# Performance work log

Hardware: AMD Instinct MI355X
Metric: run time of the kernel (lower is better)

The kernel has to match this reference:

```python
import jax, jax.numpy as jnp
import numpy as np

HEAD_SIZE = 64


def q_shift_multihead(x, ph, pw, head_dim=HEAD_SIZE, shift=1):
    # x: [B, T, C], T == ph*pw. Quarter-wise spatial shifts per head channel block.
    B, T, C = x.shape
    a = jnp.transpose(x, (0, 2, 1)).reshape(B, C // head_dim, head_dim, ph, pw)
    q = head_dim // 4
    out = jnp.zeros_like(a)
    out = out.at[:, :, 0:q, :, shift:].set(a[:, :, 0:q, :, :-shift])          # shift right in W
    out = out.at[:, :, q:2 * q, :, :-shift].set(a[:, :, q:2 * q, :, shift:])  # shift left in W
    out = out.at[:, :, 2 * q:3 * q, shift:, :].set(a[:, :, 2 * q:3 * q, :-shift, :])  # shift down in H
    out = out.at[:, :, 3 * q:, :-shift, :].set(a[:, :, 3 * q:, shift:, :])            # shift up in H
    return jnp.transpose(out.reshape(B, C, T), (0, 2, 1))


def wkv6(r, k, v, w, u):
    # RWKV-6 linear recurrence. r,k,v,w: [B,T,C]; u: [H, hs]. Decay applied as exp(-exp(w)).
    B, T, C = r.shape
    H, hs = C // HEAD_SIZE, HEAD_SIZE
    rh = jnp.transpose(r.reshape(B, T, H, hs), (1, 0, 2, 3))
    kh = jnp.transpose(k.reshape(B, T, H, hs), (1, 0, 2, 3))
    vh = jnp.transpose(v.reshape(B, T, H, hs), (1, 0, 2, 3))
    wh = jnp.exp(-jnp.exp(jnp.transpose(w.reshape(B, T, H, hs), (1, 0, 2, 3))))

    def step(S, inp):  # S: [B,H,hs(key j),hs(val i)]
        rt, kt, vt, wt = inp
        kv = kt[..., :, None] * vt[..., None, :]                # [B,H,hs,hs]
        y = jnp.einsum('bhj,bhji->bhi', rt, S + u[None, :, :, None] * kv)
        return wt[..., None] * S + kv, y

    S0 = jnp.zeros((B, H, hs, hs), r.dtype)
    _, ys = jax.lax.scan(step, S0, (rh, kh, vh, wh))
    return jnp.transpose(ys, (1, 0, 2, 3)).reshape(B, T, C)


def group_norm(x, weight, bias, n_groups, eps=1e-5):
    # x: [N, C]
    N, C = x.shape
    g = x.reshape(N, n_groups, C // n_groups)
    mu = g.mean(-1, keepdims=True)
    var = ((g - mu) ** 2).mean(-1, keepdims=True)
    g = (g - mu) / jnp.sqrt(var + eps)
    return g.reshape(N, C) * weight + bias


def setup_inputs() -> dict:
    key = jax.random.key(0)
    B, ph, pw, C = 8, 32, 32, 768
    T = ph * pw
    n_layer, layer_id = 12, 6
    H = C // HEAD_SIZE
    ks = jax.random.split(key, 10)
    x = jax.random.normal(ks[0], (B, T, C), jnp.float32)
    W_r = 0.02 * jax.random.normal(ks[1], (C, C), jnp.float32)
    W_k = 0.02 * jax.random.normal(ks[2], (C, C), jnp.float32)
    W_v = 0.02 * jax.random.normal(ks[3], (C, C), jnp.float32)
    W_g = 0.02 * jax.random.normal(ks[4], (C, C), jnp.float32)
    W_o = 0.02 * jax.random.normal(ks[5], (C, C), jnp.float32)
    r01 = layer_id / (n_layer - 1)
    r10 = 1.0 - layer_id / n_layer
    ddd = np.arange(C, dtype=np.float64) / C
    maa_x = jnp.asarray(1.0 - ddd ** r10, jnp.float32).reshape(1, 1, C)
    maa_w = maa_x
    maa_k = maa_x
    maa_v = jnp.asarray(1.0 - (ddd ** r10 + 0.3 * r01), jnp.float32).reshape(1, 1, C)
    maa_r = jnp.asarray(1.0 - ddd ** (0.5 * r10), jnp.float32).reshape(1, 1, C)
    maa_g = maa_r
    maa_w1 = jax.random.uniform(ks[6], (C, 32 * 5), jnp.float32, -1e-4, 1e-4)
    maa_w2 = jax.random.uniform(ks[7], (5, 32, C), jnp.float32, -1e-4, 1e-4)
    n = np.arange(C, dtype=np.float64)
    time_decay = jnp.asarray(-6 + 5 * (n / (C - 1)) ** (0.7 + 1.3 * r01), jnp.float32).reshape(1, 1, C)
    dec_w1 = jax.random.uniform(ks[8], (C, 64), jnp.float32, -1e-4, 1e-4)
    dec_w2 = jax.random.uniform(ks[9], (64, C), jnp.float32, -1e-4, 1e-4)
    zig = ((n + 1) % 3 - 1) * 0.1
    faaaa = jnp.asarray(r01 * (1 - n / (C - 1)) + zig, jnp.float32).reshape(H, HEAD_SIZE)
    ln_w = jnp.ones((C,), jnp.float32)
    ln_b = jnp.zeros((C,), jnp.float32)
    return dict(x=x, W_r=W_r, W_k=W_k, W_v=W_v, W_g=W_g, W_o=W_o,
                maa_x=maa_x, maa_w=maa_w, maa_k=maa_k, maa_v=maa_v, maa_r=maa_r, maa_g=maa_g,
                maa_w1=maa_w1, maa_w2=maa_w2, time_decay=time_decay,
                dec_w1=dec_w1, dec_w2=dec_w2, faaaa=faaaa, ln_w=ln_w, ln_b=ln_b,
                patch_h=ph, patch_w=pw)


def reference(x, W_r, W_k, W_v, W_g, W_o, maa_x, maa_w, maa_k, maa_v, maa_r, maa_g,
              maa_w1, maa_w2, time_decay, dec_w1, dec_w2, faaaa, ln_w, ln_b,
              patch_h, patch_w):
    B, T, C = x.shape
    xx = q_shift_multihead(x, patch_h, patch_w) - x
    xxx = x + xx * maa_x
    t = jnp.tanh(xxx @ maa_w1).reshape(B, T, 5, 32)
    m = jnp.einsum('btfr,frc->fbtc', t, maa_w2)  # [5,B,T,C]
    mw, mk, mv, mr, mg = m[0], m[1], m[2], m[3], m[4]
    xw = x + xx * (maa_w + mw)
    xk = x + xx * (maa_k + mk)
    xv = x + xx * (maa_v + mv)
    xr = x + xx * (maa_r + mr)
    xg = x + xx * (maa_g + mg)
    r = xr @ W_r.T
    k = xk @ W_k.T
    v = xv @ W_v.T
    g = jax.nn.relu(xg @ W_g.T)
    ww = jnp.tanh(xw @ dec_w1) @ dec_w2
    w = time_decay + ww
    y = wkv6(r, k, v, w, faaaa)
    y = group_norm(y.reshape(B * T, C), ln_w, ln_b, C // HEAD_SIZE).reshape(B, T, C)
    return (y * g) @ W_o.T
```

## Files before the change

### kernel.cpp

```cpp
#include <hip/hip_runtime.h>
#include <math.h>


#define EPI_NONE 0
#define EPI_TANH 1
#define EPI_RELU 2
#define EPI_BIAS 3

typedef float f32x4 __attribute__((ext_vector_type(4)));
typedef __bf16 bf16x8 __attribute__((ext_vector_type(8)));

__device__ __forceinline__ ushort f2bf(float x) {
  unsigned u = __float_as_uint(x);
  return (ushort)((u + 0x7fffu + ((u >> 16) & 1u)) >> 16);
}

#define GLDS16(gp, lp)                                                   \
  __builtin_amdgcn_global_load_lds(                                      \
      (const __attribute__((address_space(1))) void*)(gp),               \
      (__attribute__((address_space(3))) void*)(lp), 16, 0, 0)

__global__ __launch_bounds__(256) void k_qshift(
    const float* __restrict__ x, const float* __restrict__ maa_x,
    float* __restrict__ xx, ushort* __restrict__ xxx_bf,
    int B, int T, int C, int ph, int pw) {
  long idx = (long)blockIdx.x * blockDim.x + threadIdx.x;
  long total = (long)B * T * C;
  if (idx >= total) return;
  int c = (int)(idx % C);
  long bt = idx / C;
  int t = (int)(bt % T);
  int quarter = (c & 63) >> 4;
  int hh = t / pw;
  int ww = t - hh * pw;
  long rowbase = (bt - t) * C;
  float sval = 0.f;
  int st = -1;
  if (quarter == 0)      { if (ww >= 1)      st = t - 1;  }
  else if (quarter == 1) { if (ww < pw - 1)  st = t + 1;  }
  else if (quarter == 2) { if (hh >= 1)      st = t - pw; }
  else                   { if (hh < ph - 1)  st = t + pw; }
  if (st >= 0) sval = x[rowbase + (long)st * C + c];
  float xval = x[idx];
  float d = sval - xval;
  xx[idx] = d;
  xxx_bf[idx] = f2bf(xval + d * maa_x[c]);
}

__global__ __launch_bounds__(256) void k_w1t(
    const float* __restrict__ w1, ushort* __restrict__ out) {
  int n = blockIdx.y;
  int k = blockIdx.x * 256 + threadIdx.x;
  float v = (n < 160) ? w1[(size_t)k * 160 + n] : 0.f;
  out[(size_t)n * 768 + k] = f2bf(v);
}

__global__ __launch_bounds__(256) void k_w2t(
    const float* __restrict__ w2, ushort* __restrict__ w2T) {
  int idx = blockIdx.x * 256 + threadIdx.x;
  int c = idx / 160, kk = idx - c * 160;
  w2T[idx] = f2bf(w2[(size_t)kk * 768 + c]);
}

__global__ __launch_bounds__(256) void k_decT(
    const float* __restrict__ w1, const float* __restrict__ w2,
    ushort* __restrict__ w1dT, ushort* __restrict__ w2dT) {
  int idx = blockIdx.x * 256 + threadIdx.x;
  if (idx < 128 * 768) {
    int n = idx / 768, k = idx - n * 768;
    float v = (n < 64) ? w1[(size_t)k * 64 + n] : 0.f;
    w1dT[idx] = f2bf(v);
  } else {
    int j = idx - 128 * 768;
    int n = j >> 6, k = j & 63;
    w2dT[j] = f2bf(w2[(size_t)k * 768 + n]);
  }
}

__global__ __launch_bounds__(256) void k_mix5m(
    const ushort* __restrict__ t5b, const ushort* __restrict__ w2T,
    const float* __restrict__ x, const float* __restrict__ xx,
    const float* __restrict__ maa_w, const float* __restrict__ maa_k,
    const float* __restrict__ maa_v, const float* __restrict__ maa_r,
    const float* __restrict__ maa_g,
    ushort* __restrict__ xw, ushort* __restrict__ xk, ushort* __restrict__ xvb,
    ushort* __restrict__ xr, ushort* __restrict__ xg, int C) {
  int tid = threadIdx.x;
  int lane = tid & 63, wid = tid >> 6;
  int m0 = blockIdx.y * 64, n0 = blockIdx.x * 128;
  int lm = lane & 15, lk = (lane >> 4) * 8;
  int rq = (lane >> 4) * 4;
  const ushort* ap = t5b + (size_t)(m0 + wid * 16 + lm) * 160 + lk;

  float xh[8][4], dh[8][4];
#pragma unroll
  for (int j = 0; j < 8; j++)
#pragma unroll
    for (int q = 0; q < 4; q++) {
      size_t off = (size_t)(m0 + wid * 16 + rq + q) * C + (n0 + j * 16 + lm);
      xh[j][q] = x[off];
      dh[j][q] = xx[off];
    }

#pragma unroll
  for (int f = 0; f < 5; f++) {
    bf16x8 af = *(const bf16x8*)(ap + f * 32);
    f32x4 acc[8];
#pragma unroll
    for (int j = 0; j < 8; j++) {
      bf16x8 bfj = *(const bf16x8*)(w2T +
          (size_t)(n0 + j * 16 + lm) * 160 + f * 32 + lk);
      acc[j] = __builtin_amdgcn_mfma_f32_16x16x32_bf16(
          af, bfj, (f32x4){0.f, 0.f, 0.f, 0.f}, 0, 0, 0);
    }
    const float* maa_f = (f == 0) ? maa_w : (f == 1) ? maa_k
                        : (f == 2) ? maa_v : (f == 3) ? maa_r : maa_g;
    ushort* dst = (f == 0) ? xw : (f == 1) ? xk
                 : (f == 2) ? xvb : (f == 3) ? xr : xg;
#pragma unroll
    for (int j = 0; j < 8; j++) {
      float mf = maa_f[n0 + j * 16 + lm];
#pragma unroll
      for (int q = 0; q < 4; q++) {
        size_t off = (size_t)(m0 + wid * 16 + rq + q) * C + (n0 + j * 16 + lm);
        dst[off] = f2bf(xh[j][q] + dh[j][q] * (mf + acc[j][q]));
      }
    }
  }
}

__global__ __launch_bounds__(256) void k_cvt5(
    const float* __restrict__ s0, const float* __restrict__ s1,
    const float* __restrict__ s2, const float* __restrict__ s3,
    const float* __restrict__ s4,
    ushort* __restrict__ d0, ushort* __restrict__ d1,
    ushort* __restrict__ d2, ushort* __restrict__ d3,
    ushort* __restrict__ d4, int n) {
  const float* s;
  ushort* d;
  switch (blockIdx.y) {
    case 0: s = s0; d = d0; break;
    case 1: s = s1; d = d1; break;
    case 2: s = s2; d = d2; break;
    case 3: s = s3; d = d3; break;
    default: s = s4; d = d4; break;
  }
  int i = (blockIdx.x * 256 + threadIdx.x) * 4;
  if (i >= n) return;
  float4 v = *(const float4*)(s + i);
  ushort4 o;
  o.x = f2bf(v.x); o.y = f2bf(v.y); o.z = f2bf(v.z); o.w = f2bf(v.w);
  *(ushort4*)(d + i) = o;
}

template <int EPI, bool NMASK, bool OBF16>
__global__ __launch_bounds__(256) void k_gemm_bf(
    const ushort* __restrict__ A, const ushort* __restrict__ W,
    const float* __restrict__ bias, void* __restrict__ Cm,
    int M, int N, int K) {
  __shared__ ushort Al[128 * 64];
  __shared__ ushort Bl[128 * 64];
  int nwg = gridDim.x * gridDim.y;
  int bid = blockIdx.y * gridDim.x + blockIdx.x;
  int swz = (nwg & 7) == 0 ? ((bid & 7) * (nwg >> 3) + (bid >> 3)) : bid;
  int bx = swz % gridDim.x, by = swz / gridDim.x;
  int m0 = by * 128, n0 = bx * 128;
  int tid = threadIdx.x;
  int lane = tid & 63, wave = tid >> 6;
  int wm = (wave >> 1) * 64, wn = (wave & 1) * 64;
  int lm = lane & 15, g = lane >> 4;
  f32x4 acc[4][4];
#pragma unroll
  for (int i = 0; i < 4; i++)
#pragma unroll
    for (int j = 0; j < 4; j++) acc[i][j] = (f32x4){0.f, 0.f, 0.f, 0.f};

  for (int k0 = 0; k0 < K; k0 += 64) {
#pragma unroll
    for (int i = 0; i < 4; i++) {
      int cid = tid + i * 256;
      int row = cid >> 3, p = cid & 7;
      int cq = p ^ (row & 7);
      GLDS16(A + (size_t)(m0 + row) * K + k0 + cq * 8, Al + cid * 8);
      GLDS16(W + (size_t)(n0 + row) * K + k0 + cq * 8, Bl + cid * 8);
    }
    __syncthreads();
#pragma unroll
    for (int s = 0; s < 2; s++) {
      bf16x8 af[4], bf[4];
#pragma unroll
      for (int i = 0; i < 4; i++) {
        int r = wm + i * 16 + lm;
        af[i] = *(const bf16x8*)&Al[r * 64 + (((s * 4 + g) ^ (r & 7)) * 8)];
        int rb = wn + i * 16 + lm;
        bf[i] = *(const bf16x8*)&Bl[rb * 64 + (((s * 4 + g) ^ (rb & 7)) * 8)];
      }
#pragma unroll
      for (int i = 0; i < 4; i++)
#pragma unroll
        for (int j = 0; j < 4; j++)
          acc[i][j] = __builtin_amdgcn_mfma_f32_16x16x32_bf16(
              af[i], bf[j], acc[i][j], 0, 0, 0);
    }
    __syncthreads();
  }
  int rq = (lane >> 4) * 4;
#pragma unroll
  for (int i = 0; i < 4; i++) {
#pragma unroll
    for (int j = 0; j < 4; j++) {
      int gn = n0 + wn + j * 16 + lm;
      if (NMASK && gn >= N) continue;
      float bv = (EPI == EPI_BIAS) ? bias[gn] : 0.f;
#pragma unroll
      for (int q = 0; q < 4; q++) {
        int gm = m0 + wm + i * 16 + rq + q;
        float val = acc[i][j][q];
        if (EPI == EPI_BIAS) val += bv;
        if (EPI == EPI_RELU) val = fmaxf(val, 0.f);
        if (EPI == EPI_TANH) val = tanhf(val);
        if (OBF16) ((ushort*)Cm)[(size_t)gm * N + gn] = f2bf(val);
        else       ((float*)Cm)[(size_t)gm * N + gn] = val;
      }
    }
  }
}

__global__ __launch_bounds__(256) void k_proj4(
    const ushort* __restrict__ A0, const ushort* __restrict__ A1,
    const ushort* __restrict__ A2, const ushort* __restrict__ A3,
    const ushort* __restrict__ W0, const ushort* __restrict__ W1,
    const ushort* __restrict__ W2, const ushort* __restrict__ W3,
    float* __restrict__ C0, float* __restrict__ C1,
    float* __restrict__ C2, float* __restrict__ C3,
    int M, int N, int K) {
  int nwg = gridDim.x;
  int bid = blockIdx.x;
  int swz = (bid & 7) * (nwg >> 3) + (bid >> 3);
  int nxt = N / 128;
  int per_z = (M / 128) * nxt;
  int z = swz / per_z;
  int rem = swz - z * per_z;
  int my = rem / nxt, nx = rem - my * nxt;
  const ushort* A = (z == 0) ? A0 : (z == 1) ? A1 : (z == 2) ? A2 : A3;
  const ushort* W = (z == 0) ? W0 : (z == 1) ? W1 : (z == 2) ? W2 : W3;
  float* Cm       = (z == 0) ? C0 : (z == 1) ? C1 : (z == 2) ? C2 : C3;
  __shared__ ushort Al[128 * 64];
  __shared__ ushort Bl[128 * 64];
  int tid = threadIdx.x;
  int m0 = my * 128, n0 = nx * 128;
  int lane = tid & 63, wave = tid >> 6;
  int wm = (wave >> 1) * 64, wn = (wave & 1) * 64;
  int lm = lane & 15, g = lane >> 4;
  f32x4 acc[4][4];
#pragma unroll
  for (int i = 0; i < 4; i++)
#pragma unroll
    for (int j = 0; j < 4; j++) acc[i][j] = (f32x4){0.f, 0.f, 0.f, 0.f};

  for (int k0 = 0; k0 < K; k0 += 64) {
#pragma unroll
    for (int i = 0; i < 4; i++) {
      int cid = tid + i * 256;
      int row = cid >> 3, p = cid & 7;
      int cq = p ^ (row & 7);
      GLDS16(A + (size_t)(m0 + row) * K + k0 + cq * 8, Al + cid * 8);
      GLDS16(W + (size_t)(n0 + row) * K + k0 + cq * 8, Bl + cid * 8);
    }
    __syncthreads();
#pragma unroll
    for (int s = 0; s < 2; s++) {
      bf16x8 af[4], bf[4];
#pragma unroll
      for (int i = 0; i < 4; i++) {
        int r = wm + i * 16 + lm;
        af[i] = *(const bf16x8*)&Al[r * 64 + (((s * 4 + g) ^ (r & 7)) * 8)];
        int rb = wn + i * 16 + lm;
        bf[i] = *(const bf16x8*)&Bl[rb * 64 + (((s * 4 + g) ^ (rb & 7)) * 8)];
      }
#pragma unroll
      for (int i = 0; i < 4; i++)
#pragma unroll
        for (int j = 0; j < 4; j++)
          acc[i][j] = __builtin_amdgcn_mfma_f32_16x16x32_bf16(
              af[i], bf[j], acc[i][j], 0, 0, 0);
    }
    __syncthreads();
  }
  bool relu = (z == 3);
  int rq = (lane >> 4) * 4;
#pragma unroll
  for (int i = 0; i < 4; i++) {
#pragma unroll
    for (int j = 0; j < 4; j++) {
      int gn = n0 + wn + j * 16 + lm;
#pragma unroll
      for (int q = 0; q < 4; q++) {
        int gm = m0 + wm + i * 16 + rq + q;
        float val = acc[i][j][q];
        if (relu) val = fmaxf(val, 0.f);
        Cm[(size_t)gm * N + gn] = val;
      }
    }
  }
}

__global__ __launch_bounds__(64) void k_wkv_pre(
    const float* __restrict__ r, const float* __restrict__ k,
    const float* __restrict__ w, const float* __restrict__ u,
    float* __restrict__ rt, float* __restrict__ kt,
    float* __restrict__ aL, float* __restrict__ pdiag,
    int B, int T, int C, int H, int L) {
  __shared__ float pls[64 * 65];
  int nch = T / L;
  int blk = blockIdx.x;
  int bh = blk / nch, c = blk - bh * nch;
  int b = bh / H, h = bh - b * H;
  int j = threadIdx.x;
  float uj = u[h * 64 + j];
  float cum = 0.f;
  long base = ((long)b * T + (long)c * L) * C + h * 64 + j;
  for (int tau = 0; tau < L; tau++) {
    long off = base + (long)tau * C;
    float wv = w[off];
    float rv = r[off];
    float kv = k[off];
    float e = expf(wv);
    rt[off] = rv * expf(-cum);
    cum += e;
    kt[off] = kv * expf(cum);
    pls[tau * 65 + j] = rv * uj * kv;
  }
  aL[((long)bh * nch + c) * 64 + j] = expf(-cum);
  __syncthreads();
  float s0 = 0.f, s1 = 0.f, s2 = 0.f, s3 = 0.f;
#pragma unroll
  for (int q = 0; q < 16; q++) {
    float4 p4 = *(const float4*)(pls + j * 65 + q * 4);
    s0 += p4.x; s1 += p4.y; s2 += p4.z; s3 += p4.w;
  }
  pdiag[(long)bh * T + c * L + j] = (s0 + s1) + (s2 + s3);
}

__global__ __launch_bounds__(256) void k_wkv_kv(
    const float* __restrict__ kt, const float* __restrict__ v,
    float* __restrict__ kvb, int B, int T, int C, int H, int L) {
  int nch = T / L;
  int blk = blockIdx.x;
  int bh = blk / nch, c = blk - bh * nch;
  int b = bh / H, h = bh - b * H;
  __shared__ float Ks[64 * 64];
  __shared__ float Vs[64 * 64];
  int tid = threadIdx.x;
  int lane = tid & 63, jg = tid >> 6;
  long cbase = ((long)b * T + (long)c * L) * C + h * 64;
#pragma unroll
  for (int i = 0; i < 4; i++) {
    int chunk = jg * 4 + i;
    int row = chunk * 4 + (lane >> 4);
    int cq = lane & 15;
    GLDS16(kt + cbase + (long)row * C + cq * 4, Ks + chunk * 256);
    GLDS16(v + cbase + (long)row * C + cq * 4, Vs + chunk * 256);
  }
  __syncthreads();
  float acc[16];
#pragma unroll
  for (int q = 0; q < 16; q++) acc[q] = 0.f;
  for (int s = 0; s < 64; s++) {
    float vi = Vs[s * 64 + lane];
#pragma unroll
    for (int q4 = 0; q4 < 4; q4++) {
      float4 kk = *(const float4*)(Ks + s * 64 + jg * 16 + q4 * 4);
      acc[q4 * 4 + 0] = fmaf(kk.x, vi, acc[q4 * 4 + 0]);
      acc[q4 * 4 + 1] = fmaf(kk.y, vi, acc[q4 * 4 + 1]);
      acc[q4 * 4 + 2] = fmaf(kk.z, vi, acc[q4 * 4 + 2]);
      acc[q4 * 4 + 3] = fmaf(kk.w, vi, acc[q4 * 4 + 3]);
    }
  }
  float* out = kvb + ((long)bh * nch + c) * 4096;
#pragma unroll
  for (int q = 0; q < 16; q++) out[(jg * 16 + q) * 64 + lane] = acc[q];
}

__global__ __launch_bounds__(256) void k_wkv_scan(
    const float* __restrict__ kvb, const float* __restrict__ aL,
    float* __restrict__ Scb, int nch) {
  int bh = blockIdx.x >> 4;
  int e = ((blockIdx.x & 15) << 8) + threadIdx.x;
  float S = 0.f;
  for (int c = 0; c < nch; c++) {
    long cb = ((long)bh * nch + c) * 4096 + e;
    Scb[cb] = S;
    S = aL[((long)bh * nch + c) * 64 + (e >> 6)] * (S + kvb[cb]);
  }
}

__global__ __launch_bounds__(256, 4) void k_wkv_intra(
    const float* __restrict__ rt, const float* __restrict__ kt,
    const float* __restrict__ v, const float* __restrict__ pdiag,
    const float* __restrict__ Scb, const float* __restrict__ g,
    const float* __restrict__ ln_w, const float* __restrict__ ln_b,
    ushort* __restrict__ z, int B, int T, int C, int H, int L) {
  int nch = T / L;
  int blk = blockIdx.x;
  int bh = blk / nch, c = blk - bh * nch;
  int b = bh / H, h = bh - b * H;
  __shared__ float TA[64 * 64];
  __shared__ float TB[64 * 64];
  int tid = threadIdx.x;
  int lane = tid & 63, wid = tid >> 6;
  int tau = lane;
  long cbase = ((long)b * T + (long)c * L) * C + h * 64;
  const float* scp = Scb + ((long)bh * nch + c) * 4096;

#pragma unroll
  for (int i = 0; i < 4; i++) {
    int chunk = wid * 4 + i;
    int row = chunk * 4 + (lane >> 4);
    int cq = lane & 15;
    GLDS16(rt + cbase + (long)row * C + ((cq ^ (row & 15)) * 4),
           TA + chunk * 256);
    GLDS16(kt + cbase + (long)row * C + cq * 4, TB + chunk * 256);
  }
  __syncthreads();

  float4 rreg[16];
#pragma unroll
  for (int q = 0; q < 16; q++)
    rreg[q] = *(const float4*)(TA + tau * 64 + ((q ^ (tau & 15)) * 4));
  float pd = pdiag[(long)bh * T + c * L + tau];
  __syncthreads();

#pragma unroll
  for (int i = 0; i < 4; i++) {
    int chunk = wid * 4 + i;
    int row = chunk * 4 + (lane >> 4);
    GLDS16(v + cbase + (long)row * C + (lane & 15) * 4, TA + chunk * 256);
  }

#pragma unroll 2
  for (int ss = 0; ss < 16; ss++) {
    int s = wid * 16 + ss;
    float a0 = 0.f, a1 = 0.f, a2 = 0.f, a3 = 0.f;
#pragma unroll
    for (int q = 0; q < 16; q++) {
      float4 kk = *(const float4*)(TB + s * 64 + q * 4);
      a0 = fmaf(rreg[q].x, kk.x, a0);
      a1 = fmaf(rreg[q].y, kk.y, a1);
      a2 = fmaf(rreg[q].z, kk.z, a2);
      a3 = fmaf(rreg[q].w, kk.w, a3);
    }
    float a = (a0 + a1) + (a2 + a3);
    float val = (s < tau) ? a : (s == tau ? pd : 0.f);
    TB[s * 64 + tau] = val;
  }
  __syncthreads();

  int row0 = wid * 16 + ((lane >> 4) << 2);
  int c0 = (lane & 15) * 4;
  float4 acc0 = {0.f, 0.f, 0.f, 0.f};
  float4 acc1 = {0.f, 0.f, 0.f, 0.f};
  float4 acc2 = {0.f, 0.f, 0.f, 0.f};
  float4 acc3 = {0.f, 0.f, 0.f, 0.f};
#define FMA1(A, P, V4)                 \
  A.x = fmaf(P, V4.x, A.x);            \
  A.y = fmaf(P, V4.y, A.y);            \
  A.z = fmaf(P, V4.z, A.z);            \
  A.w = fmaf(P, V4.w, A.w);
#pragma unroll 4
  for (int j = 0; j < 64; j++) {
    float4 pp = *(const float4*)(TB + j * 64 + row0);
    float4 vv = *(const float4*)(TA + j * 64 + c0);
    FMA1(acc0, pp.x, vv);
    FMA1(acc1, pp.y, vv);
    FMA1(acc2, pp.z, vv);
    FMA1(acc3, pp.w, vv);
  }
  __syncthreads();

#define WRQ(SG)                                                          \
  {                                                                      \
    _Pragma("unroll") for (int qq = 0; qq < 16; qq++) {                  \
      const float* rp = (const float*)&rreg[(SG) * 4 + (qq >> 2)];       \
      TA[((SG) * 16 + qq) * 64 + tau] = rp[qq & 3];                      \
    }                                                                    \
  }
  if (wid == 0)      WRQ(0)
  else if (wid == 1) WRQ(1)
  else if (wid == 2) WRQ(2)
  else               WRQ(3)
#undef WRQ
  __syncthreads();

#pragma unroll 4
  for (int j = 0; j < 64; j++) {
    float4 rr = *(const float4*)(TA + j * 64 + row0);
    float4 ssv = *(const float4*)(scp + j * 64 + c0);
    FMA1(acc0, rr.x, ssv);
    FMA1(acc1, rr.y, ssv);
    FMA1(acc2, rr.z, ssv);
    FMA1(acc3, rr.w, ssv);
  }
#undef FMA1

  float4 lw4 = *(const float4*)(ln_w + h * 64 + c0);
  float4 lb4 = *(const float4*)(ln_b + h * 64 + c0);
#define GNROW(A, m)                                                        \
  {                                                                        \
    float s1 = (A.x + A.y) + (A.z + A.w);                                  \
    s1 += __shfl_xor(s1, 1, 64);                                           \
    s1 += __shfl_xor(s1, 2, 64);                                           \
    s1 += __shfl_xor(s1, 4, 64);                                           \
    s1 += __shfl_xor(s1, 8, 64);                                           \
    float mu = s1 * (1.f / 64.f);                                          \
    float4 dd;                                                             \
    dd.x = A.x - mu; dd.y = A.y - mu; dd.z = A.z - mu; dd.w = A.w - mu;    \
    float s2 = (dd.x * dd.x + dd.y * dd.y) + (dd.z * dd.z + dd.w * dd.w);  \
    s2 += __shfl_xor(s2, 1, 64);                                           \
    s2 += __shfl_xor(s2, 2, 64);                                           \
    s2 += __shfl_xor(s2, 4, 64);                                           \
    s2 += __shfl_xor(s2, 8, 64);                                           \
    float rstd = rsqrtf(s2 * (1.f / 64.f) + 1e-5f);                        \
    long off = cbase + (long)(row0 + m) * C + c0;                          \
    float4 g4 = *(const float4*)(g + off);                                 \
    ushort4 ob;                                                            \
    ob.x = f2bf((dd.x * rstd * lw4.x + lb4.x) * g4.x);                     \
    ob.y = f2bf((dd.y * rstd * lw4.y + lb4.y) * g4.y);                     \
    ob.z = f2bf((dd.z * rstd * lw4.z + lb4.z) * g4.z);                     \
    ob.w = f2bf((dd.w * rstd * lw4.w + lb4.w) * g4.w);                     \
    *(ushort4*)(z + off) = ob;                                             \
  }
  GNROW(acc0, 0)
  GNROW(acc1, 1)
  GNROW(acc2, 2)
  GNROW(acc3, 3)
#undef GNROW
}

extern "C" void kernel_launch(void* const* d_in, const int* in_sizes, int n_in,
                              void* d_out, int out_size, void* d_ws, size_t ws_size,
                              hipStream_t stream) {
  const int B = 8, T = 1024, C = 768, H = 12, ph = 32, pw = 32;
  const int M = B * T;
  const int L = 64, NCH = T / L;

  const float* x        = (const float*)d_in[0];
  const float* W_r      = (const float*)d_in[1];
  const float* W_k      = (const float*)d_in[2];
  const float* W_v      = (const float*)d_in[3];
  const float* W_g      = (const float*)d_in[4];
  const float* W_o      = (const float*)d_in[5];
  const float* maa_x    = (const float*)d_in[6];
  const float* maa_w    = (const float*)d_in[7];
  const float* maa_k    = (const float*)d_in[8];
  const float* maa_v    = (const float*)d_in[9];
  const float* maa_r    = (const float*)d_in[10];
  const float* maa_g    = (const float*)d_in[11];
  const float* maa_w1   = (const float*)d_in[12];
  const float* maa_w2   = (const float*)d_in[13];
  const float* time_dec = (const float*)d_in[14];
  const float* dec_w1   = (const float*)d_in[15];
  const float* dec_w2   = (const float*)d_in[16];
  const float* faaaa    = (const float*)d_in[17];
  const float* ln_w     = (const float*)d_in[18];
  const float* ln_b     = (const float*)d_in[19];

  float* ws = (float*)d_ws;
  const size_t S = (size_t)M * C;
  float* F0 = ws + 0 * S;
  float* F1 = ws + 1 * S;
  float* F2 = ws + 2 * S;
  float* F3 = ws + 3 * S;
  float* F4 = ws + 4 * S;
  float* F5 = ws + 5 * S;
  float* F6 = ws + 6 * S;
  float* t5    = ws + 7 * S;
  float* t6    = t5 + (size_t)M * 160;
  float* aLb   = t6 + (size_t)M * 64;
  float* pdiag = aLb + (size_t)B * H * NCH * 64;
  float* dec_t = pdiag + (size_t)B * H * T;

  ushort* xxx_bf = (ushort*)F1;
  ushort* xw_bf = (ushort*)F2;
  ushort* xr_bf = (ushort*)F5;
  ushort* xk_bf = xr_bf + S;
  ushort* xv_bf = (ushort*)F6;
  ushort* xg_bf = xv_bf + S;
  ushort* z_bf  = (ushort*)F6;
  ushort* t5b   = (ushort*)t5;
  ushort* t_bf  = (ushort*)dec_t;
  ushort* w2T   = t_bf + (size_t)M * 64;
  float* kvb = F0;
  float* Scb = F1;
  const int WSZ = C * C;
  ushort* wr_bf = (ushort*)t5;
  ushort* wk_bf = wr_bf + WSZ;
  ushort* wv_bf = wk_bf + WSZ;
  ushort* wg_bf = wv_bf + WSZ;
  ushort* wo_bf = (ushort*)t6;
  ushort* maa1T = wo_bf + WSZ;
  ushort* w1dT  = maa1T + 256 * 768;
  ushort* w2dT  = w1dT + 128 * 768;

  {
    long total = (long)M * C;
    k_qshift<<<(int)((total + 255) / 256), 256, 0, stream>>>(
        x, maa_x, F0, xxx_bf, B, T, C, ph, pw);
  }
  {
    dim3 gt(3, 256);
    k_w1t<<<gt, 256, 0, stream>>>(maa_w1, maa1T);
    k_w2t<<<768 * 160 / 256, 256, 0, stream>>>(maa_w2, w2T);
    k_decT<<<(128 * 768 + 768 * 64) / 256, 256, 0, stream>>>(
        dec_w1, dec_w2, w1dT, w2dT);
    dim3 grid(2, M / 128);
    k_gemm_bf<EPI_TANH, true, true><<<grid, 256, 0, stream>>>(
        xxx_bf, maa1T, nullptr, t5b, M, 160, C);
  }
  {
    dim3 grid(C / 128, M / 64);
    k_mix5m<<<grid, 256, 0, stream>>>(t5b, w2T, x, F0, maa_w, maa_k, maa_v,
                                      maa_r, maa_g, xw_bf, xk_bf, xv_bf, xr_bf,
                                      xg_bf, C);
  }
  {
    dim3 grid((WSZ / 4 + 255) / 256, 5);
    k_cvt5<<<grid, 256, 0, stream>>>(W_r, W_k, W_v, W_g, W_o,
                                     wr_bf, wk_bf, wv_bf, wg_bf, wo_bf, WSZ);
  }
  {
    k_proj4<<<(C / 128) * (M / 128) * 4, 256, 0, stream>>>(
        xr_bf, xk_bf, xv_bf, xg_bf, wr_bf, wk_bf, wv_bf, wg_bf,
        F0, F1, F3, F4, M, C, C);
  }
  {
    dim3 g1(1, M / 128);
    k_gemm_bf<EPI_TANH, true, true><<<g1, 256, 0, stream>>>(
        xw_bf, w1dT, nullptr, t_bf, M, 64, C);
    dim3 g2(C / 128, M / 128);
    k_gemm_bf<EPI_BIAS, false, false><<<g2, 256, 0, stream>>>(
        t_bf, w2dT, time_dec, F2, M, C, 64);
  }
  k_wkv_pre<<<B * H * NCH, 64, 0, stream>>>(F0, F1, F2, faaaa, F5, F2,
                                            aLb, pdiag, B, T, C, H, L);
  k_wkv_kv<<<B * H * NCH, 256, 0, stream>>>(F2, F3, kvb, B, T, C, H, L);
  k_wkv_scan<<<B * H * 16, 256, 0, stream>>>(kvb, aLb, Scb, NCH);
  k_wkv_intra<<<B * H * NCH, 256, 0, stream>>>(F5, F2, F3, pdiag, Scb, F4,
                                               ln_w, ln_b, z_bf, B, T, C, H, L);
  {
    dim3 grid(C / 128, M / 128);
    k_gemm_bf<EPI_NONE, false, false><<<grid, 256, 0, stream>>>(
        z_bf, wo_bf, nullptr, (float*)d_out, M, C, C);
  }
}
```

Measured before the change: 442.0 us.

## Recompute shift diff in mix kernel, merge weight prep kernels, tune wkv occupancy

The qshift kernel no longer writes the fp32 xx tensor. k_mix5m instead recomputes the shifted difference from x using per-row neighbour indices, which avoids a large fp32 write and re-read at the cost of extra gathered loads of x. The three weight transpose/convert kernels are merged into one launch to cut launch overhead. k_wkv_intra gets a higher launch-bounds occupancy hint and s_setprio around its FMA loops, which may add register pressure or spills.

```diff
diff --git a/kernel.cpp b/kernel.cpp
--- a/kernel.cpp
+++ b/kernel.cpp
@@ -22,7 +22,7 @@
 
 __global__ __launch_bounds__(256) void k_qshift(
     const float* __restrict__ x, const float* __restrict__ maa_x,
-    float* __restrict__ xx, ushort* __restrict__ xxx_bf,
+    ushort* __restrict__ xxx_bf,
     int B, int T, int C, int ph, int pw) {
   long idx = (long)blockIdx.x * blockDim.x + threadIdx.x;
   long total = (long)B * T * C;
@@ -43,48 +43,42 @@
   if (st >= 0) sval = x[rowbase + (long)st * C + c];
   float xval = x[idx];
   float d = sval - xval;
-  xx[idx] = d;
   xxx_bf[idx] = f2bf(xval + d * maa_x[c]);
 }
 
-__global__ __launch_bounds__(256) void k_w1t(
-    const float* __restrict__ w1, ushort* __restrict__ out) {
-  int n = blockIdx.y;
-  int k = blockIdx.x * 256 + threadIdx.x;
-  float v = (n < 160) ? w1[(size_t)k * 160 + n] : 0.f;
-  out[(size_t)n * 768 + k] = f2bf(v);
-}
-
-__global__ __launch_bounds__(256) void k_w2t(
-    const float* __restrict__ w2, ushort* __restrict__ w2T) {
-  int idx = blockIdx.x * 256 + threadIdx.x;
-  int c = idx / 160, kk = idx - c * 160;
-  w2T[idx] = f2bf(w2[(size_t)kk * 768 + c]);
-}
-
-__global__ __launch_bounds__(256) void k_decT(
+__global__ __launch_bounds__(256) void k_wprep(
     const float* __restrict__ w1, const float* __restrict__ w2,
+    const float* __restrict__ dw1, const float* __restrict__ dw2,
+    ushort* __restrict__ maa1T, ushort* __restrict__ w2T,
     ushort* __restrict__ w1dT, ushort* __restrict__ w2dT) {
   int idx = blockIdx.x * 256 + threadIdx.x;
-  if (idx < 128 * 768) {
+  if (idx < 196608) {
     int n = idx / 768, k = idx - n * 768;
-    float v = (n < 64) ? w1[(size_t)k * 64 + n] : 0.f;
-    w1dT[idx] = f2bf(v);
+    maa1T[idx] = f2bf(n < 160 ? w1[(size_t)k * 160 + n] : 0.f);
+  } else if (idx < 196608 + 122880) {
+    int j = idx - 196608;
+    int c = j / 160, kk = j - c * 160;
+    w2T[j] = f2bf(w2[(size_t)kk * 768 + c]);
+  } else if (idx < 196608 + 122880 + 98304) {
+    int j = idx - (196608 + 122880);
+    int n = j / 768, k = j - n * 768;
+    w1dT[j] = f2bf(n < 64 ? dw1[(size_t)k * 64 + n] : 0.f);
   } else {
-    int j = idx - 128 * 768;
+    int j = idx - (196608 + 122880 + 98304);
     int n = j >> 6, k = j & 63;
-    w2dT[j] = f2bf(w2[(size_t)k * 768 + n]);
+    w2dT[j] = f2bf(dw2[(size_t)k * 768 + n]);
   }
 }
 
 __global__ __launch_bounds__(256) void k_mix5m(
     const ushort* __restrict__ t5b, const ushort* __restrict__ w2T,
-    const float* __restrict__ x, const float* __restrict__ xx,
+    const float* __restrict__ x,
     const float* __restrict__ maa_w, const float* __restrict__ maa_k,
     const float* __restrict__ maa_v, const float* __restrict__ maa_r,
     const float* __restrict__ maa_g,
     ushort* __restrict__ xw, ushort* __restrict__ xk, ushort* __restrict__ xvb,
-    ushort* __restrict__ xr, ushort* __restrict__ xg, int C) {
+    ushort* __restrict__ xr, ushort* __restrict__ xg,
+    int C, int T, int ph, int pw) {
   int tid = threadIdx.x;
   int lane = tid & 63, wid = tid >> 6;
   int m0 = blockIdx.y * 64, n0 = blockIdx.x * 128;
@@ -92,14 +86,30 @@
   int rq = (lane >> 4) * 4;
   const ushort* ap = t5b + (size_t)(m0 + wid * 16 + lm) * 160 + lk;
 
+  int stq[4][4];
+#pragma unroll
+  for (int q = 0; q < 4; q++) {
+    int mr = m0 + wid * 16 + rq + q;
+    int t = mr % T;
+    int hh = t / pw, ww = t - hh * pw;
+    stq[q][0] = (ww >= 1)      ? mr - 1  : -1;
+    stq[q][1] = (ww < pw - 1)  ? mr + 1  : -1;
+    stq[q][2] = (hh >= 1)      ? mr - pw : -1;
+    stq[q][3] = (hh < ph - 1)  ? mr + pw : -1;
+  }
+
   float xh[8][4], dh[8][4];
 #pragma unroll
   for (int j = 0; j < 8; j++)
 #pragma unroll
     for (int q = 0; q < 4; q++) {
-      size_t off = (size_t)(m0 + wid * 16 + rq + q) * C + (n0 + j * 16 + lm);
-      xh[j][q] = x[off];
-      dh[j][q] = xx[off];
+      int mr = m0 + wid * 16 + rq + q;
+      int col = n0 + j * 16 + lm;
+      float xv = x[(size_t)mr * C + col];
+      int sr = stq[q][j & 3];
+      float sv = (sr >= 0) ? x[(size_t)sr * C + col] : 0.f;
+      xh[j][q] = xv;
+      dh[j][q] = sv - xv;
     }
 
 #pragma unroll
@@ -395,7 +405,7 @@
   }
 }
 
-__global__ __launch_bounds__(256, 4) void k_wkv_intra(
+__global__ __launch_bounds__(256, 5) void k_wkv_intra(
     const float* __restrict__ rt, const float* __restrict__ kt,
     const float* __restrict__ v, const float* __restrict__ pdiag,
     const float* __restrict__ Scb, const float* __restrict__ g,
@@ -438,6 +448,7 @@
     GLDS16(v + cbase + (long)row * C + (lane & 15) * 4, TA + chunk * 256);
   }
 
+  __builtin_amdgcn_s_setprio(1);
 #pragma unroll 2
   for (int ss = 0; ss < 16; ss++) {
     int s = wid * 16 + ss;
@@ -454,6 +465,7 @@
     float val = (s < tau) ? a : (s == tau ? pd : 0.f);
     TB[s * 64 + tau] = val;
   }
+  __builtin_amdgcn_s_setprio(0);
   __syncthreads();
 
   int row0 = wid * 16 + ((lane >> 4) << 2);
@@ -467,6 +479,7 @@
   A.y = fmaf(P, V4.y, A.y);            \
   A.z = fmaf(P, V4.z, A.z);            \
   A.w = fmaf(P, V4.w, A.w);
+  __builtin_amdgcn_s_setprio(1);
 #pragma unroll 4
   for (int j = 0; j < 64; j++) {
     float4 pp = *(const float4*)(TB + j * 64 + row0);
@@ -476,6 +489,7 @@
     FMA1(acc2, pp.z, vv);
     FMA1(acc3, pp.w, vv);
   }
+  __builtin_amdgcn_s_setprio(0);
   __syncthreads();
 
 #define WRQ(SG)                                                          \
@@ -492,6 +506,7 @@
 #undef WRQ
   __syncthreads();
 
+  __builtin_amdgcn_s_setprio(1);
 #pragma unroll 4
   for (int j = 0; j < 64; j++) {
     float4 rr = *(const float4*)(TA + j * 64 + row0);
@@ -501,6 +516,7 @@
     FMA1(acc2, rr.z, ssv);
     FMA1(acc3, rr.w, ssv);
   }
+  __builtin_amdgcn_s_setprio(0);
 #undef FMA1
 
   float4 lw4 = *(const float4*)(ln_w + h * 64 + c0);
@@ -605,23 +621,20 @@
   {
     long total = (long)M * C;
     k_qshift<<<(int)((total + 255) / 256), 256, 0, stream>>>(
-        x, maa_x, F0, xxx_bf, B, T, C, ph, pw);
+        x, maa_x, xxx_bf, B, T, C, ph, pw);
   }
   {
-    dim3 gt(3, 256);
-    k_w1t<<<gt, 256, 0, stream>>>(maa_w1, maa1T);
-    k_w2t<<<768 * 160 / 256, 256, 0, stream>>>(maa_w2, w2T);
-    k_decT<<<(128 * 768 + 768 * 64) / 256, 256, 0, stream>>>(
-        dec_w1, dec_w2, w1dT, w2dT);
+    k_wprep<<<1824, 256, 0, stream>>>(maa_w1, maa_w2, dec_w1, dec_w2,
+                                      maa1T, w2T, w1dT, w2dT);
     dim3 grid(2, M / 128);
     k_gemm_bf<EPI_TANH, true, true><<<grid, 256, 0, stream>>>(
         xxx_bf, maa1T, nullptr, t5b, M, 160, C);
   }
   {
     dim3 grid(C / 128, M / 64);
-    k_mix5m<<<grid, 256, 0, stream>>>(t5b, w2T, x, F0, maa_w, maa_k, maa_v,
+    k_mix5m<<<grid, 256, 0, stream>>>(t5b, w2T, x, maa_w, maa_k, maa_v,
                                       maa_r, maa_g, xw_bf, xk_bf, xv_bf, xr_bf,
-                                      xg_bf, C);
+                                      xg_bf, C, T, ph, pw);
   }
   {
     dim3 grid((WSZ / 4 + 255) / 256, 5);
```

After: 417.1 us. 5.6% less time.
